# Kernel optimization log

Measured on AMD Instinct MI355X. Metric: run time of the kernel, lower is better.

## Reference

```python
import jax, jax.numpy as jnp
import numpy as np

B = 2048        # batch
D_IN = 512      # input_dim
H = 768         # hidden_dim
A = 5001        # num_atoms
RULE_LEN = 4
N_DATA = 56000.0


def setup_inputs() -> dict:
    key = jax.random.key(0)
    ks = jax.random.split(key, 24)
    def w(k, shape, fan):
        return (jax.random.normal(k, shape, jnp.float32) / np.sqrt(fan)).astype(jnp.float32)
    return {
        'x': jax.random.normal(ks[0], (B, D_IN), jnp.float32),
        'x_mask': jax.random.randint(ks[1], (B, A), 0, 2, jnp.int32),
        # linear_base: Linear(512,768) ReLU Linear(768,768) ReLU Linear(768,768)
        'W1': w(ks[2], (H, D_IN), D_IN), 'b1': jnp.zeros((H,), jnp.float32),
        'W2': w(ks[3], (H, H), H),       'b2': jnp.zeros((H,), jnp.float32),
        'W3': w(ks[4], (H, H), H),       'b3': jnp.zeros((H,), jnp.float32),
        # single-layer GRU (input H, hidden H); gates ordered r,z,n as in torch
        'W_ih': w(ks[5], (3 * H, H), H), 'b_ih': jnp.zeros((3 * H,), jnp.float32),
        'W_hh': w(ks[6], (3 * H, H), H), 'b_hh': jnp.zeros((3 * H,), jnp.float32),
        # gru_head: Linear(H, num_atoms)
        'Wh': w(ks[7], (A, H), H), 'bh': jnp.zeros((A,), jnp.float32),
        # atom embedding table
        'ae_weight': jax.random.normal(ks[8], (A, H), jnp.float32) * 0.02,
        # stand-in consequent estimator heads (mu, coverage)
        'w_mu': w(ks[9], (H, 1), H),  'b_mu': jnp.zeros((1,), jnp.float32),
        'w_cov': w(ks[10], (H, 1), H), 'b_cov': jnp.zeros((1,), jnp.float32),
        'alpha': jnp.ones((1,), jnp.float32),
    }


def _gru_step(xt, h, W_ih, b_ih, W_hh, b_hh):
    gi = xt @ W_ih.T + b_ih
    gh = h @ W_hh.T + b_hh
    i_r, i_z, i_n = jnp.split(gi, 3, axis=-1)
    h_r, h_z, h_n = jnp.split(gh, 3, axis=-1)
    r = jax.nn.sigmoid(i_r + h_r)
    z = jax.nn.sigmoid(i_z + h_z)
    n = jnp.tanh(i_n + r * h_n)
    return (1.0 - z) * n + z * h


def reference(x, x_mask, W1, b1, W2, b2, W3, b3, W_ih, b_ih, W_hh, b_hh,
              Wh, bh, ae_weight, w_mu, b_mu, w_cov, b_cov, alpha):
    # base (dnn) encoder -> cls embedding [B, H]
    cls = jax.nn.relu(x @ W1.T + b1)
    cls = jax.nn.relu(cls @ W2.T + b2)
    cls = cls @ W3.T + b3

    ae_det = jax.lax.stop_gradient(ae_weight)  # ae.weight is always detached in the original
    mask = x_mask.astype(jnp.float32)
    h = jnp.zeros_like(cls)
    cur = cls
    probs = []
    idx = None
    gkey = jax.random.key(42)
    batch_idx = jnp.arange(cls.shape[0])

    for j in range(RULE_LEN):
        h = _gru_step(cur, h, W_ih, b_ih, W_hh, b_hh)  # dropout = identity (eval)
        logits = h @ Wh.T + bh  # [B, A]
        if j == 0:
            row_zero = jnp.sum(mask, axis=1) == 0.0
            mask = mask.at[:, 0].set(jnp.where(row_zero, 1.0, mask[:, 0]))
        else:
            mask = jnp.where((idx == 0)[:, None], 0.0, mask)
            mask = mask.at[:, 0].set(1.0)
        masked = jnp.where(mask > 0.0, logits, -jnp.inf)
        # gumbel-softmax, tau=1, hard=True (straight-through)
        u = jax.random.uniform(jax.random.fold_in(gkey, j), masked.shape,
                               jnp.float32, 1e-6, 1.0 - 1e-6)
        g = -jnp.log(-jnp.log(u))
        y_soft = jax.nn.softmax(masked + g, axis=1)
        idx = jnp.argmax(y_soft, axis=1)
        y_hard = jax.nn.one_hot(idx, A, dtype=y_soft.dtype)
        prob = y_hard + y_soft - jax.lax.stop_gradient(y_soft)
        probs.append(prob)
        # scatter zero at the selected atom so it can't repeat
        mask = mask.at[batch_idx, idx].set(0.0)
        cur = cls + prob @ ae_det  # [B, H]

    atom_prob = jnp.stack(probs, axis=1)  # [B, rule_len, A]
    atoms = jnp.einsum('bra,ad->brd', atom_prob, ae_det)  # [B, rule_len, H]

    # stand-in consequent estimator: (mu, coverage) from summed atoms
    a = jnp.sum(atoms, axis=1)
    mu = jax.nn.sigmoid(a @ w_mu + b_mu)[:, 0]
    coverage = jax.nn.sigmoid(a @ w_cov + b_cov)[:, 0]

    n = coverage * N_DATA
    inv = alpha[0] / n
    pp = (mu + inv) / (1.0 + 2.0 * inv)
    cp = jnp.stack([1.0 - pp, pp], axis=-1)  # [B, 2]
    out = jnp.log(cp)  # head=1 -> mean over heads is identity
    return (out, atom_prob, cp)
```

## Files before the change

### kernel.cpp

```cpp
#include <hip/hip_runtime.h>
#include <stdint.h>
#include <math.h>

#define B_    2048
#define DIN_  512
#define H_    768
#define G3_   2304
#define A_    5001
#define APAD_ 5120
#define RL_   4
#define NDATA_ 56000.0f

typedef _Float16 f16x8 __attribute__((ext_vector_type(8)));
typedef _Float16 f16x4 __attribute__((ext_vector_type(4)));
typedef float    f32x4 __attribute__((ext_vector_type(4)));

__host__ __device__ __forceinline__ void threefry2x32(
    uint32_t k0, uint32_t k1, uint32_t x0, uint32_t x1,
    uint32_t* o0, uint32_t* o1)
{
  const uint32_t ks2 = k0 ^ k1 ^ 0x1BD11BDAu;
#define TF_R(r) { x0 += x1; x1 = (x1 << (r)) | (x1 >> (32 - (r))); x1 ^= x0; }
  x0 += k0; x1 += k1;
  TF_R(13) TF_R(15) TF_R(26) TF_R(6)
  x0 += k1;  x1 += ks2 + 1u;
  TF_R(17) TF_R(29) TF_R(16) TF_R(24)
  x0 += ks2; x1 += k0 + 2u;
  TF_R(13) TF_R(15) TF_R(26) TF_R(6)
  x0 += k0;  x1 += k1 + 3u;
  TF_R(17) TF_R(29) TF_R(16) TF_R(24)
  x0 += k1;  x1 += ks2 + 4u;
  TF_R(13) TF_R(15) TF_R(26) TF_R(6)
  x0 += ks2; x1 += k0 + 5u;
#undef TF_R
  *o0 = x0; *o1 = x1;
}

__device__ __forceinline__ float gumbel_for(uint32_t k0, uint32_t k1, uint32_t n)
{
  uint32_t o0, o1;
  threefry2x32(k0, k1, 0u, n, &o0, &o1);
  const uint32_t bits = o0 ^ o1;
  const float f = __uint_as_float((bits >> 9) | 0x3f800000u);
  const float minv = 1e-6f;
  const float maxv = 1.0f - 1e-6f;
  const float span = maxv - minv;
  float u = __fmul_rn(f, span);
  u = __fadd_rn(u, minv);
  u = __fsub_rn(u, span);
  u = fmaxf(minv, u);
  return -logf(-logf(u));
}

struct HL { _Float16 h, l; };
__device__ __forceinline__ HL split64(float v)
{
  HL r;
  const float s = v * 64.f;
  r.h = (_Float16)s;
  r.l = (_Float16)(s - (float)r.h);
  return r;
}

__device__ __forceinline__ void gload16(const void* g, void* l)
{
  __builtin_amdgcn_global_load_lds(
      (const __attribute__((address_space(1))) void*)g,
      (__attribute__((address_space(3))) void*)l, 16, 0, 0);
}

struct PSJobs {
  const float* src[7];
  _Float16* hi[7];
  _Float16* lo[7];
  int R[7]; int K[7];
  int cum[8];
};

__global__ __launch_bounds__(256)
void presplit_all(PSJobs J)
{
  const int g = blockIdx.x * 256 + threadIdx.x;
  if (g >= J.cum[7]) return;
  int j = 0;
  while (g >= J.cum[j + 1]) ++j;
  const int i = g - J.cum[j];
  const int K = J.K[j];
  const int e = i * 4;
  const int row = e / K;
  float4 f = make_float4(0.f, 0.f, 0.f, 0.f);
  if (row < J.R[j]) f = *(const float4*)(J.src[j] + (size_t)row * K + (e - row * K));
  const HL s0 = split64(f.x), s1 = split64(f.y);
  const HL s2 = split64(f.z), s3 = split64(f.w);
  const f16x4 hv = {s0.h, s1.h, s2.h, s3.h};
  ((f16x4*)J.hi[j])[i] = hv;
  if (J.lo[j]) {
    const f16x4 lv = {s0.l, s1.l, s2.l, s3.l};
    ((f16x4*)J.lo[j])[i] = lv;
  }
}

__global__ __launch_bounds__(256)
void prep_k(const int* __restrict__ xmask, uint8_t* __restrict__ mask,
            const float* __restrict__ Wh, float* __restrict__ wmaxsq,
            const float* __restrict__ x, _Float16* __restrict__ xh,
            _Float16* __restrict__ xl)
{
  const int blk = blockIdx.x, tid = threadIdx.x;
  __shared__ float redf[256];
  __shared__ int   redi[256];
  if (blk < B_) {
    const int b = blk;
    int s = 0;
    for (int a = tid; a < A_; a += 256) {
      const int m = (xmask[(size_t)b * A_ + a] != 0) ? 1 : 0;
      mask[(size_t)b * A_ + a] = (uint8_t)m;
      s += m;
    }
    redi[tid] = s; __syncthreads();
    for (int t = 128; t > 0; t >>= 1) {
      if (tid < t) redi[tid] += redi[tid + t];
      __syncthreads();
    }
    if (tid == 0 && redi[0] == 0) mask[(size_t)b * A_] = 1;
  } else if (blk < B_ + A_) {
    const int a = blk - B_;
    float p = 0.f;
    for (int d = tid; d < H_; d += 256) {
      const float w = Wh[(size_t)a * H_ + d];
      p += w * w;
    }
    redf[tid] = p; __syncthreads();
    for (int t = 128; t > 0; t >>= 1) {
      if (tid < t) redf[tid] += redf[tid + t];
      __syncthreads();
    }
    if (tid == 0) atomicMax((int*)wmaxsq, __float_as_int(redf[0]));
  } else {
    const int i = (blk - B_ - A_) * 256 + tid;
    const int n4 = B_ * DIN_ / 4;
    if (i < n4) {
      const float4 f = ((const float4*)x)[i];
      const HL s0 = split64(f.x), s1 = split64(f.y);
      const HL s2 = split64(f.z), s3 = split64(f.w);
      const f16x4 hv = {s0.h, s1.h, s2.h, s3.h};
      const f16x4 lv = {s0.l, s1.l, s2.l, s3.l};
      ((f16x4*)xh)[i] = hv;
      ((f16x4*)xl)[i] = lv;
    }
  }
}

struct GJob {
  const _Float16 *Ah, *Al, *Bh, *Bl;
  const float* bias;
  float* C;
  _Float16 *Ch, *Cl;
  int M, K, ldc, n0, Nv;
  int npass, act, wsplit, gum;
};
struct GArgs { GJob j[2]; int sx; uint32_t k0, k1; };

__global__ __launch_bounds__(256)
void gemm2job(GArgs P)
{
  __shared__ _Float16 sA[2][128 * 32];
  __shared__ _Float16 sB[2][128 * 32];

  const int jid = (blockIdx.x < P.sx) ? 0 : 1;
  const GJob J = P.j[jid];
  const int bxx = blockIdx.x - (jid ? P.sx : 0);
  const int bm = blockIdx.y * 128;
  if (bm >= J.M) return;
  const int bn = J.n0 + bxx * 128;

  const int tid = threadIdx.x;
  const int lane = tid & 63, wave = tid >> 6;
  const int wx = wave & 1, wy = wave >> 1;
  const int q = lane >> 4, mr = lane & 15;
  const int K = J.K;
  const int np3 = (J.npass == 3);

  auto stage = [&](int k0) {
#pragma unroll
    for (int t = 0; t < 2; ++t) {
      const int c = wave * 2 + t;
      const int row = c * 16 + (lane >> 2);
      const int kc = (lane & 3) * 8;
      const size_t ga = (size_t)(bm + row) * K + k0 + kc;
      const size_t gb = (size_t)(bn + row) * K + k0 + kc;
      gload16(J.Ah + ga, &sA[0][c * 512]);
      gload16(J.Bh + gb, &sB[0][c * 512]);
      if (np3) {
        gload16(J.Al + ga, &sA[1][c * 512]);
        gload16(J.Bl + gb, &sB[1][c * 512]);
      }
    }
  };

  f32x4 acc[4][4];
#pragma unroll
  for (int i = 0; i < 4; ++i)
#pragma unroll
    for (int j = 0; j < 4; ++j) acc[i][j] = (f32x4)0.f;

  stage(0);
  const int T = K / 32;
  const int abase = (wy * 64 + mr) * 32 + q * 8;
  const int bbase = (wx * 64 + mr) * 32 + q * 8;

  for (int t = 0; t < T; ++t) {
    __syncthreads();
    f16x8 ah[4], al[4], bhv[4], blv[4];
#pragma unroll
    for (int mi = 0; mi < 4; ++mi) {
      ah[mi]  = *(const f16x8*)&sA[0][abase + mi * 512];
      bhv[mi] = *(const f16x8*)&sB[0][bbase + mi * 512];
    }
    if (np3) {
#pragma unroll
      for (int mi = 0; mi < 4; ++mi) {
        al[mi]  = *(const f16x8*)&sA[1][abase + mi * 512];
        blv[mi] = *(const f16x8*)&sB[1][bbase + mi * 512];
      }
    }
    __syncthreads();
    if (t + 1 < T) stage((t + 1) * 32);

    if (np3) {
#pragma unroll
      for (int ni = 0; ni < 4; ++ni)
#pragma unroll
        for (int mi = 0; mi < 4; ++mi) {
          acc[mi][ni] = __builtin_amdgcn_mfma_f32_16x16x32_f16(ah[mi], bhv[ni], acc[mi][ni], 0, 0, 0);
          acc[mi][ni] = __builtin_amdgcn_mfma_f32_16x16x32_f16(al[mi], bhv[ni], acc[mi][ni], 0, 0, 0);
          acc[mi][ni] = __builtin_amdgcn_mfma_f32_16x16x32_f16(ah[mi], blv[ni], acc[mi][ni], 0, 0, 0);
        }
    } else {
#pragma unroll
      for (int ni = 0; ni < 4; ++ni)
#pragma unroll
        for (int mi = 0; mi < 4; ++mi)
          acc[mi][ni] = __builtin_amdgcn_mfma_f32_16x16x32_f16(ah[mi], bhv[ni], acc[mi][ni], 0, 0, 0);
    }
  }

  const float sc = 1.f / 4096.f;
#pragma unroll
  for (int ni = 0; ni < 4; ++ni) {
    const int n = bn + wx * 64 + ni * 16 + mr;
    if (n >= J.Nv) continue;
    const float bv = J.bias ? J.bias[n] : 0.f;
#pragma unroll
    for (int mi = 0; mi < 4; ++mi) {
      const int m0 = bm + wy * 64 + mi * 16 + q * 4;
#pragma unroll
      for (int r = 0; r < 4; ++r) {
        const int m = m0 + r;
        float v = acc[mi][ni][r] * sc + bv;
        if (J.act) v = fmaxf(v, 0.f);
        if (J.gum) v += gumbel_for(P.k0, P.k1, (uint32_t)(m * J.ldc + n));
        const size_t off = (size_t)m * J.ldc + n;
        if (J.C) J.C[off] = v;
        if (J.wsplit) {
          const HL s = split64(v);
          J.Ch[off] = s.h;
          J.Cl[off] = s.l;
        }
      }
    }
  }
}

__global__ __launch_bounds__(256)
void gru_elem(const float* __restrict__ gi, const float* __restrict__ bhh,
              float* __restrict__ h, _Float16* __restrict__ hh_,
              _Float16* __restrict__ hl_)
{
  const int i = blockIdx.x * 256 + threadIdx.x;
  if (i >= B_ * H_) return;
  const int b = i / H_;
  const int d = i - b * H_;
  const float* gib = gi + (size_t)b * G3_;
  const float ir = gib[d], iz = gib[H_ + d], in_ = gib[2 * H_ + d];
  const float hr = bhh[d], hz = bhh[H_ + d], hn = bhh[2 * H_ + d];
  const float r = 1.f / (1.f + expf(-(ir + hr)));
  const float z = 1.f / (1.f + expf(-(iz + hz)));
  const float n = tanhf(in_ + r * hn);
  const float hv = (1.f - z) * n;
  h[i] = hv;
  const HL s = split64(hv);
  hh_[i] = s.h; hl_[i] = s.l;
}

__global__ __launch_bounds__(256)
void select_step(const float* __restrict__ v, uint8_t* __restrict__ mask,
                 int* __restrict__ idxs, const float* __restrict__ giCls,
                 const float* __restrict__ AeWih, float* __restrict__ atomp,
                 float* __restrict__ hbuf, const float* __restrict__ WhF,
                 const float* __restrict__ bh, const float* __restrict__ wmaxsq,
                 const float* __restrict__ gh, const float* __restrict__ bhh,
                 _Float16* __restrict__ hh_, _Float16* __restrict__ hl_,
                 uint32_t k0, uint32_t k1, int step)
{
  const int b = blockIdx.x, tid = threadIdx.x;
  uint8_t* mrow = mask + (size_t)b * A_;
  __shared__ float vsh[A_];
  __shared__ float hsh[H_];
  __shared__ float gish[G3_];
  __shared__ float sv[256];
  __shared__ int   si[256];
  __shared__ int   s_list[64];
  __shared__ int   s_n;
  __shared__ int   s_sel;

  float hp = 0.f;
  for (int d = tid; d < H_; d += 256) {
    const float t = hbuf[(size_t)b * H_ + d];
    hsh[d] = t; hp += t * t;
  }
  sv[tid] = hp; __syncthreads();
  for (int t = 128; t > 0; t >>= 1) {
    if (tid < t) sv[tid] += sv[tid + t];
    __syncthreads();
  }
  const float hn2 = sv[0];
  __syncthreads();

  if (step > 0) {
    const int prev = idxs[(step - 1) * B_ + b];
    if (prev == 0)
      for (int a = tid; a < A_; a += 256) mrow[a] = 0;
    __syncthreads();
    if (tid == 0) mrow[0] = 1;
  }
  if (tid == 0) s_n = 0;
  __syncthreads();

  const float* vrow = v + (size_t)b * A_;
  float bv = -INFINITY; int bi = A_;
  for (int a = tid; a < A_; a += 256) {
    const float val = mrow[a] ? vrow[a] : -INFINITY;
    vsh[a] = val;
    if (val > bv) { bv = val; bi = a; }
  }
  sv[tid] = bv; si[tid] = bi; __syncthreads();
  for (int t = 128; t > 0; t >>= 1) {
    if (tid < t) {
      const float v2 = sv[tid + t]; const int i2 = si[tid + t];
      if (v2 > sv[tid] || (v2 == sv[tid] && i2 < si[tid])) { sv[tid] = v2; si[tid] = i2; }
    }
    __syncthreads();
  }
  const float amax = sv[0];
  __syncthreads();

  const float delta = 2.0f * 0.0009765625f * sqrtf(hn2 * wmaxsq[0]);
  const float thr = amax - 2.f * delta;

  for (int a = tid; a < A_; a += 256)
    if (vsh[a] >= thr) {
      const int p = atomicAdd(&s_n, 1);
      if (p < 64) s_list[p] = a;
    }
  __syncthreads();
  const int nc = (s_n < 64) ? s_n : 64;

  const uint32_t nbase = (uint32_t)b * (uint32_t)A_;
  float best = -INFINITY; int bestA = A_;
  for (int c = 0; c < nc; ++c) {
    const int a = s_list[c];
    const float* wr = WhF + (size_t)a * H_;
    float p = 0.f;
    for (int d = tid; d < H_; d += 256) p += hsh[d] * wr[d];
    sv[tid] = p; __syncthreads();
    for (int t = 128; t > 0; t >>= 1) {
      if (tid < t) sv[tid] += sv[tid + t];
      __syncthreads();
    }
    if (tid == 0) {
      const float ev = sv[0] + bh[a] + gumbel_for(k0, k1, nbase + (uint32_t)a);
      if (ev > best || (ev == best && a < bestA)) { best = ev; bestA = a; }
    }
    __syncthreads();
  }
  if (tid == 0) {
    s_sel = bestA;
    mrow[bestA] = 0;
    idxs[step * B_ + b] = bestA;
    atomp[(size_t)b * (RL_ * A_) + (size_t)step * A_ + bestA] = 1.0f;
  }
  __syncthreads();

  if (step < RL_ - 1) {
    const int sel = s_sel;
    const float* ar = AeWih + (size_t)sel * G3_;
    const float* gr = giCls + (size_t)b * G3_;
    for (int d = tid; d < G3_; d += 256) gish[d] = gr[d] + ar[d];
    __syncthreads();
    const float* ghb = gh + (size_t)b * G3_;
    for (int d = tid; d < H_; d += 256) {
      const float r = 1.f / (1.f + expf(-(gish[d] + ghb[d])));
      const float z = 1.f / (1.f + expf(-(gish[H_ + d] + ghb[H_ + d])));
      const float n = tanhf(gish[2 * H_ + d] + r * ghb[2 * H_ + d]);
      const float hv = (1.f - z) * n + z * hsh[d];
      hbuf[(size_t)b * H_ + d] = hv;
      const HL s = split64(hv);
      hh_[(size_t)b * H_ + d] = s.h;
      hl_[(size_t)b * H_ + d] = s.l;
    }
  }
}

__global__ __launch_bounds__(256)
void head_k(const int* __restrict__ idxs, const float* __restrict__ ae,
            const float* __restrict__ w_mu, const float* __restrict__ b_mu,
            const float* __restrict__ w_cov, const float* __restrict__ b_cov,
            const float* __restrict__ alpha, float* __restrict__ outf)
{
  const int b = blockIdx.x, tid = threadIdx.x;
  const int i0 = idxs[0 * B_ + b], i1 = idxs[1 * B_ + b];
  const int i2 = idxs[2 * B_ + b], i3 = idxs[3 * B_ + b];
  const float* r0 = ae + (size_t)i0 * H_;
  const float* r1 = ae + (size_t)i1 * H_;
  const float* r2 = ae + (size_t)i2 * H_;
  const float* r3 = ae + (size_t)i3 * H_;
  float pmu = 0.f, pcv = 0.f;
  for (int d = tid; d < H_; d += 256) {
    const float a = r0[d] + r1[d] + r2[d] + r3[d];
    pmu += a * w_mu[d];
    pcv += a * w_cov[d];
  }
  __shared__ float smu[256], scv[256];
  smu[tid] = pmu; scv[tid] = pcv;
  __syncthreads();
  for (int s = 128; s > 0; s >>= 1) {
    if (tid < s) { smu[tid] += smu[tid + s]; scv[tid] += scv[tid + s]; }
    __syncthreads();
  }
  if (tid == 0) {
    const float mu = 1.f / (1.f + expf(-(smu[0] + b_mu[0])));
    const float cv = 1.f / (1.f + expf(-(scv[0] + b_cov[0])));
    const float n = cv * NDATA_;
    const float inv = alpha[0] / n;
    const float pp = (mu + inv) / (1.f + 2.f * inv);
    outf[2 * b + 0] = logf(1.f - pp);
    outf[2 * b + 1] = logf(pp);
    float* cp = outf + 2 * B_ + (size_t)B_ * RL_ * A_;
    cp[2 * b + 0] = 1.f - pp;
    cp[2 * b + 1] = pp;
  }
}

extern "C" void kernel_launch(void* const* d_in, const int* in_sizes, int n_in,
                              void* d_out, int out_size, void* d_ws, size_t ws_size,
                              hipStream_t stream)
{
  const float* x     = (const float*)d_in[0];
  const int*   xmask = (const int*)d_in[1];
  const float* W1 = (const float*)d_in[2];  const float* b1 = (const float*)d_in[3];
  const float* W2 = (const float*)d_in[4];  const float* b2 = (const float*)d_in[5];
  const float* W3 = (const float*)d_in[6];  const float* b3 = (const float*)d_in[7];
  const float* Wih = (const float*)d_in[8]; const float* bih = (const float*)d_in[9];
  const float* Whh = (const float*)d_in[10];const float* bhh = (const float*)d_in[11];
  const float* Wh = (const float*)d_in[12]; const float* bh = (const float*)d_in[13];
  const float* ae = (const float*)d_in[14];
  const float* w_mu = (const float*)d_in[15];  const float* b_mu = (const float*)d_in[16];
  const float* w_cov = (const float*)d_in[17]; const float* b_cov = (const float*)d_in[18];
  const float* alpha = (const float*)d_in[19];

  char* ws = (char*)d_ws;
  size_t off = 0;
  auto alloc = [&](size_t bytes) -> void* {
    void* p = ws + off;
    off += (bytes + 255) & ~(size_t)255;
    return p;
  };
  float* hbuf   = (float*)alloc((size_t)B_ * H_ * 4);
  float* giCls  = (float*)alloc((size_t)B_ * G3_ * 4);
  float* gh     = (float*)alloc((size_t)B_ * G3_ * 4);
  float* vbuf   = (float*)alloc((size_t)B_ * A_ * 4);
  float* AeWih  = (float*)alloc((size_t)APAD_ * G3_ * 4);
  uint8_t* mask = (uint8_t*)alloc((size_t)B_ * A_);
  int* idxs     = (int*)alloc((size_t)RL_ * B_ * 4);
  _Float16* hh_ = (_Float16*)alloc((size_t)B_ * H_ * 2);
  _Float16* hl_ = (_Float16*)alloc((size_t)B_ * H_ * 2);
  _Float16* clsh = (_Float16*)alloc((size_t)B_ * H_ * 2);
  _Float16* clsl = (_Float16*)alloc((size_t)B_ * H_ * 2);
  _Float16* xh  = (_Float16*)alloc((size_t)B_ * DIN_ * 2);
  _Float16* xl  = (_Float16*)alloc((size_t)B_ * DIN_ * 2);
  _Float16* t1h = (_Float16*)alloc((size_t)B_ * H_ * 2);
  _Float16* t1l = (_Float16*)alloc((size_t)B_ * H_ * 2);
  _Float16* t2h = (_Float16*)alloc((size_t)B_ * H_ * 2);
  _Float16* t2l = (_Float16*)alloc((size_t)B_ * H_ * 2);
  _Float16* w1h = (_Float16*)alloc((size_t)H_ * DIN_ * 2);
  _Float16* w1l = (_Float16*)alloc((size_t)H_ * DIN_ * 2);
  _Float16* w2h = (_Float16*)alloc((size_t)H_ * H_ * 2);
  _Float16* w2l = (_Float16*)alloc((size_t)H_ * H_ * 2);
  _Float16* w3h = (_Float16*)alloc((size_t)H_ * H_ * 2);
  _Float16* w3l = (_Float16*)alloc((size_t)H_ * H_ * 2);
  _Float16* wihh = (_Float16*)alloc((size_t)G3_ * H_ * 2);
  _Float16* wihl = (_Float16*)alloc((size_t)G3_ * H_ * 2);
  _Float16* whhh = (_Float16*)alloc((size_t)G3_ * H_ * 2);
  _Float16* whhl = (_Float16*)alloc((size_t)G3_ * H_ * 2);
  _Float16* whhi = (_Float16*)alloc((size_t)APAD_ * H_ * 2);
  _Float16* aeh  = (_Float16*)alloc((size_t)APAD_ * H_ * 2);
  _Float16* ael  = (_Float16*)alloc((size_t)APAD_ * H_ * 2);
  float* wmaxsq = (float*)alloc(4);

  float* outf  = (float*)d_out;
  float* atomp = outf + 2 * B_;

  (void)hipMemsetAsync(d_out, 0, (size_t)out_size * sizeof(float), stream);
  (void)hipMemsetAsync(wmaxsq, 0, 4, stream);

  PSJobs J;
  const float* srcs[7] = {W1, W2, W3, Wih, Whh, Wh, ae};
  _Float16* his[7] = {w1h, w2h, w3h, wihh, whhh, whhi, aeh};
  _Float16* los[7] = {w1l, w2l, w3l, wihl, whhl, nullptr, ael};
  const int Rs[7]    = {H_, H_, H_, G3_, G3_, A_, A_};
  const int Rpads[7] = {H_, H_, H_, G3_, G3_, APAD_, APAD_};
  const int Ks[7]    = {DIN_, H_, H_, H_, H_, H_, H_};
  J.cum[0] = 0;
  for (int j = 0; j < 7; ++j) {
    J.src[j] = srcs[j]; J.hi[j] = his[j]; J.lo[j] = los[j];
    J.R[j] = Rs[j]; J.K[j] = Ks[j];
    J.cum[j + 1] = J.cum[j] + Rpads[j] * Ks[j] / 4;
  }
  presplit_all<<<(J.cum[7] + 255) / 256, 256, 0, stream>>>(J);

  prep_k<<<B_ + A_ + (B_ * DIN_ / 4 + 255) / 256, 256, 0, stream>>>(
      xmask, mask, Wh, wmaxsq, x, xh, xl);

  auto mkjob = [](const _Float16* Ah, const _Float16* Al, const _Float16* Bh,
                  const _Float16* Bl, const float* bias, float* C,
                  _Float16* Ch, _Float16* Cl, int M, int K, int ldc,
                  int n0, int Nv, int npass, int act, int wsplit, int gum) {
    GJob g; g.Ah = Ah; g.Al = Al; g.Bh = Bh; g.Bl = Bl; g.bias = bias;
    g.C = C; g.Ch = Ch; g.Cl = Cl; g.M = M; g.K = K; g.ldc = ldc;
    g.n0 = n0; g.Nv = Nv; g.npass = npass; g.act = act; g.wsplit = wsplit;
    g.gum = gum;
    return g;
  };
  auto aejob = [&](int t0, int nt) {
    return mkjob(aeh, ael, wihh, wihl, nullptr, AeWih, nullptr, nullptr,
                 APAD_, H_, G3_, t0 * 128, G3_, 3, 0, 0, 0);
    (void)nt;
  };

  {
    GArgs P;
    P.j[0] = mkjob(xh, xl, w1h, w1l, b1, nullptr, t1h, t1l,
                   B_, DIN_, H_, 0, H_, 3, 1, 1, 0);
    P.j[1] = aejob(0, 5);
    P.sx = H_ / 128; P.k0 = 0; P.k1 = 0;
    gemm2job<<<dim3(H_ / 128 + 5, APAD_ / 128), 256, 0, stream>>>(P);
  }
  {
    GArgs P;
    P.j[0] = mkjob(t1h, t1l, w2h, w2l, b2, nullptr, t2h, t2l,
                   B_, H_, H_, 0, H_, 3, 1, 1, 0);
    P.j[1] = aejob(5, 5);
    P.sx = H_ / 128; P.k0 = 0; P.k1 = 0;
    gemm2job<<<dim3(H_ / 128 + 5, APAD_ / 128), 256, 0, stream>>>(P);
  }
  {
    GArgs P;
    P.j[0] = mkjob(t2h, t2l, w3h, w3l, b3, nullptr, clsh, clsl,
                   B_, H_, H_, 0, H_, 3, 0, 1, 0);
    P.j[1] = aejob(10, 4);
    P.sx = H_ / 128; P.k0 = 0; P.k1 = 0;
    gemm2job<<<dim3(H_ / 128 + 4, APAD_ / 128), 256, 0, stream>>>(P);
  }
  {
    GArgs P;
    P.j[0] = mkjob(clsh, clsl, wihh, wihl, bih, giCls, nullptr, nullptr,
                   B_, H_, G3_, 0, G3_, 3, 0, 0, 0);
    P.j[1] = aejob(14, 4);
    P.sx = G3_ / 128; P.k0 = 0; P.k1 = 0;
    gemm2job<<<dim3(G3_ / 128 + 4, APAD_ / 128), 256, 0, stream>>>(P);
  }

  uint32_t fk0[RL_], fk1[RL_];
  for (int j = 0; j < RL_; ++j)
    threefry2x32(0u, 42u, 0u, (uint32_t)j, &fk0[j], &fk1[j]);

  gru_elem<<<(B_ * H_ + 255) / 256, 256, 0, stream>>>(giCls, bhh, hbuf, hh_, hl_);

  for (int j = 0; j < RL_; ++j) {
    GArgs P;
    P.j[0] = mkjob(hh_, nullptr, whhi, nullptr, bh, vbuf, nullptr, nullptr,
                   B_, H_, A_, 0, A_, 1, 0, 0, 1);
    const int gx0 = APAD_ / 128;
    int gx = gx0;
    if (j < RL_ - 1) {
      P.j[1] = mkjob(hh_, hl_, whhh, whhl, bhh, gh, nullptr, nullptr,
                     B_, H_, G3_, 0, G3_, 3, 0, 0, 0);
      gx += G3_ / 128;
    } else {
      P.j[1] = P.j[0];
    }
    P.sx = gx0; P.k0 = fk0[j]; P.k1 = fk1[j];
    gemm2job<<<dim3(gx, B_ / 128), 256, 0, stream>>>(P);

    select_step<<<B_, 256, 0, stream>>>(vbuf, mask, idxs, giCls, AeWih, atomp,
                                        hbuf, Wh, bh, wmaxsq, gh, bhh, hh_, hl_,
                                        fk0[j], fk1[j], j);
  }

  head_k<<<B_, 256, 0, stream>>>(idxs, ae, w_mu, b_mu, w_cov, b_cov, alpha, outf);
}
```

Measured before the change: 1.082 ms.

## Load GEMM fragments directly from global memory into registers, dropping LDS staging

```diff
diff --git a/kernel.cpp b/kernel.cpp
--- a/kernel.cpp
+++ b/kernel.cpp
@@ -60,13 +60,6 @@
   r.h = (_Float16)s;
   r.l = (_Float16)(s - (float)r.h);
   return r;
-}
-
-__device__ __forceinline__ void gload16(const void* g, void* l)
-{
-  __builtin_amdgcn_global_load_lds(
-      (const __attribute__((address_space(1))) void*)g,
-      (__attribute__((address_space(3))) void*)l, 16, 0, 0);
 }
 
 struct PSJobs {
@@ -164,9 +157,6 @@
 __global__ __launch_bounds__(256)
 void gemm2job(GArgs P)
 {
-  __shared__ _Float16 sA[2][128 * 32];
-  __shared__ _Float16 sB[2][128 * 32];
-
   const int jid = (blockIdx.x < P.sx) ? 0 : 1;
   const GJob J = P.j[jid];
   const int bxx = blockIdx.x - (jid ? P.sx : 0);
@@ -180,69 +170,67 @@
   const int q = lane >> 4, mr = lane & 15;
   const int K = J.K;
   const int np3 = (J.npass == 3);
-
-  auto stage = [&](int k0) {
-#pragma unroll
-    for (int t = 0; t < 2; ++t) {
-      const int c = wave * 2 + t;
-      const int row = c * 16 + (lane >> 2);
-      const int kc = (lane & 3) * 8;
-      const size_t ga = (size_t)(bm + row) * K + k0 + kc;
-      const size_t gb = (size_t)(bn + row) * K + k0 + kc;
-      gload16(J.Ah + ga, &sA[0][c * 512]);
-      gload16(J.Bh + gb, &sB[0][c * 512]);
-      if (np3) {
-        gload16(J.Al + ga, &sA[1][c * 512]);
-        gload16(J.Bl + gb, &sB[1][c * 512]);
+  const ptrdiff_t dA = np3 ? (J.Al - J.Ah) : 0;
+  const ptrdiff_t dB = np3 ? (J.Bl - J.Bh) : 0;
+
+  const _Float16 *pa[4], *pb[4];
+#pragma unroll
+  for (int i = 0; i < 4; ++i) {
+    pa[i] = J.Ah + (size_t)(bm + wy * 64 + i * 16 + mr) * K + q * 8;
+    pb[i] = J.Bh + (size_t)(bn + wx * 64 + i * 16 + mr) * K + q * 8;
+  }
+
+  f32x4 acc[4][4];
+#pragma unroll
+  for (int i = 0; i < 4; ++i)
+#pragma unroll
+    for (int j = 0; j < 4; ++j) acc[i][j] = (f32x4)0.f;
+
+  const int T = K / 32;
+  f16x8 a0[4], b0[4], a1[4], b1[4], la[4], lb[4];
+
+#pragma unroll
+  for (int i = 0; i < 4; ++i) {
+    a0[i] = *(const f16x8*)(pa[i]);
+    b0[i] = *(const f16x8*)(pb[i]);
+  }
+
+  auto kstep = [&](int t, f16x8* ac, f16x8* bc, f16x8* an, f16x8* bn2) {
+    const int o = t * 32;
+    if (np3) {
+#pragma unroll
+      for (int i = 0; i < 4; ++i) {
+        la[i] = *(const f16x8*)(pa[i] + o + dA);
+        lb[i] = *(const f16x8*)(pb[i] + o + dB);
       }
     }
+    if (t + 1 < T) {
+      const int o1 = o + 32;
+#pragma unroll
+      for (int i = 0; i < 4; ++i) {
+        an[i]  = *(const f16x8*)(pa[i] + o1);
+        bn2[i] = *(const f16x8*)(pb[i] + o1);
+      }
+    }
+#pragma unroll
+    for (int ni = 0; ni < 4; ++ni)
+#pragma unroll
+      for (int mi = 0; mi < 4; ++mi)
+        acc[mi][ni] = __builtin_amdgcn_mfma_f32_16x16x32_f16(ac[mi], bc[ni], acc[mi][ni], 0, 0, 0);
+    if (np3) {
+#pragma unroll
+      for (int ni = 0; ni < 4; ++ni)
+#pragma unroll
+        for (int mi = 0; mi < 4; ++mi) {
+          acc[mi][ni] = __builtin_amdgcn_mfma_f32_16x16x32_f16(la[mi], bc[ni], acc[mi][ni], 0, 0, 0);
+          acc[mi][ni] = __builtin_amdgcn_mfma_f32_16x16x32_f16(ac[mi], lb[ni], acc[mi][ni], 0, 0, 0);
+        }
+    }
   };
 
-  f32x4 acc[4][4];
-#pragma unroll
-  for (int i = 0; i < 4; ++i)
-#pragma unroll
-    for (int j = 0; j < 4; ++j) acc[i][j] = (f32x4)0.f;
-
-  stage(0);
-  const int T = K / 32;
-  const int abase = (wy * 64 + mr) * 32 + q * 8;
-  const int bbase = (wx * 64 + mr) * 32 + q * 8;
-
-  for (int t = 0; t < T; ++t) {
-    __syncthreads();
-    f16x8 ah[4], al[4], bhv[4], blv[4];
-#pragma unroll
-    for (int mi = 0; mi < 4; ++mi) {
-      ah[mi]  = *(const f16x8*)&sA[0][abase + mi * 512];
-      bhv[mi] = *(const f16x8*)&sB[0][bbase + mi * 512];
-    }
-    if (np3) {
-#pragma unroll
-      for (int mi = 0; mi < 4; ++mi) {
-        al[mi]  = *(const f16x8*)&sA[1][abase + mi * 512];
-        blv[mi] = *(const f16x8*)&sB[1][bbase + mi * 512];
-      }
-    }
-    __syncthreads();
-    if (t + 1 < T) stage((t + 1) * 32);
-
-    if (np3) {
-#pragma unroll
-      for (int ni = 0; ni < 4; ++ni)
-#pragma unroll
-        for (int mi = 0; mi < 4; ++mi) {
-          acc[mi][ni] = __builtin_amdgcn_mfma_f32_16x16x32_f16(ah[mi], bhv[ni], acc[mi][ni], 0, 0, 0);
-          acc[mi][ni] = __builtin_amdgcn_mfma_f32_16x16x32_f16(al[mi], bhv[ni], acc[mi][ni], 0, 0, 0);
-          acc[mi][ni] = __builtin_amdgcn_mfma_f32_16x16x32_f16(ah[mi], blv[ni], acc[mi][ni], 0, 0, 0);
-        }
-    } else {
-#pragma unroll
-      for (int ni = 0; ni < 4; ++ni)
-#pragma unroll
-        for (int mi = 0; mi < 4; ++mi)
-          acc[mi][ni] = __builtin_amdgcn_mfma_f32_16x16x32_f16(ah[mi], bhv[ni], acc[mi][ni], 0, 0, 0);
-    }
+  for (int t = 0; t < T; t += 2) {
+    kstep(t, a0, b0, a1, b1);
+    if (t + 1 < T) kstep(t + 1, a1, b1, a0, b0);
   }
 
   const float sc = 1.f / 4096.f;
@@ -542,17 +530,16 @@
     g.gum = gum;
     return g;
   };
-  auto aejob = [&](int t0, int nt) {
+  auto aejob = [&](int t0) {
     return mkjob(aeh, ael, wihh, wihl, nullptr, AeWih, nullptr, nullptr,
                  APAD_, H_, G3_, t0 * 128, G3_, 3, 0, 0, 0);
-    (void)nt;
   };
 
   {
     GArgs P;
     P.j[0] = mkjob(xh, xl, w1h, w1l, b1, nullptr, t1h, t1l,
                    B_, DIN_, H_, 0, H_, 3, 1, 1, 0);
-    P.j[1] = aejob(0, 5);
+    P.j[1] = aejob(0);
     P.sx = H_ / 128; P.k0 = 0; P.k1 = 0;
     gemm2job<<<dim3(H_ / 128 + 5, APAD_ / 128), 256, 0, stream>>>(P);
   }
@@ -560,7 +547,7 @@
     GArgs P;
     P.j[0] = mkjob(t1h, t1l, w2h, w2l, b2, nullptr, t2h, t2l,
                    B_, H_, H_, 0, H_, 3, 1, 1, 0);
-    P.j[1] = aejob(5, 5);
+    P.j[1] = aejob(5);
     P.sx = H_ / 128; P.k0 = 0; P.k1 = 0;
     gemm2job<<<dim3(H_ / 128 + 5, APAD_ / 128), 256, 0, stream>>>(P);
   }
@@ -568,7 +555,7 @@
     GArgs P;
     P.j[0] = mkjob(t2h, t2l, w3h, w3l, b3, nullptr, clsh, clsl,
                    B_, H_, H_, 0, H_, 3, 0, 1, 0);
-    P.j[1] = aejob(10, 4);
+    P.j[1] = aejob(10);
     P.sx = H_ / 128; P.k0 = 0; P.k1 = 0;
     gemm2job<<<dim3(H_ / 128 + 4, APAD_ / 128), 256, 0, stream>>>(P);
   }
@@ -576,7 +563,7 @@
     GArgs P;
     P.j[0] = mkjob(clsh, clsl, wihh, wihl, bih, giCls, nullptr, nullptr,
                    B_, H_, G3_, 0, G3_, 3, 0, 0, 0);
-    P.j[1] = aejob(14, 4);
+    P.j[1] = aejob(14);
     P.sx = G3_ / 128; P.k0 = 0; P.k1 = 0;
     gemm2job<<<dim3(G3_ / 128 + 4, APAD_ / 128), 256, 0, stream>>>(P);
   }
```

Measured after the change: 1.509 ms. 39.4% more time.
